# Performance work log

Measured on AMD Instinct MI355X. Metric: run time of the kernel, lower is better.

## Reference

```python
import jax, jax.numpy as jnp
import numpy as np

SR = 48000
MAX_DUR = 5.0
N_AUDIO = 480000  # 10 s @ 48 kHz
K_IR = int(SR * MAX_DUR)  # 240000 taps


def setup_inputs() -> dict:
    key = jax.random.key(0)
    k1, k2 = jax.random.split(key)
    audio = jax.random.normal(k1, (N_AUDIO,), dtype=jnp.float32)
    impulse_response = jax.random.normal(k2, (K_IR,), dtype=jnp.float32)
    return {"audio": audio, "impulse_response": impulse_response}


def reference(audio, impulse_response):
    # torch: pad audio with (K-1) zeros, then conv1d (= cross-correlation, no flip)
    K = impulse_response.shape[0]
    a_pad = jnp.concatenate([audio, jnp.zeros((K - 1,), dtype=audio.dtype)])
    # out[t] = sum_k a_pad[t+k] * ir[k], valid correlation -> length N
    out = jnp.correlate(a_pad, impulse_response, mode="valid")
    # trailing peak normalization
    return out / jnp.max(jnp.abs(out))
```

## Files before the change

kernel.cpp:

```cpp
#include <hip/hip_runtime.h>

typedef unsigned int u32;


constexpr int N_AUDIO = 480000;
constexpr int M_FFT   = 1048576;

constexpr size_t OFF_C0   = 0;
constexpr size_t OFF_C1   = (size_t)M_FFT * 8;
constexpr size_t OFF_SLOT = OFF_C1 + (size_t)M_FFT * 8;

#define SW(i) ((i) + ((i) >> 4))
constexpr int LSZ = 1088;

struct F2 { float x, y; };
constexpr double D_PI = 3.14159265358979323846264338327950288;
constexpr double tay_sin(double x) {
    double t = x, s = x, x2 = x * x;
    for (int k = 1; k <= 11; ++k) { t *= -x2 / (double)((2 * k) * (2 * k + 1)); s += t; }
    return s;
}
constexpr double tay_cos(double x) {
    double t = 1.0, s = 1.0, x2 = x * x;
    for (int k = 1; k <= 11; ++k) { t *= -x2 / (double)((2 * k - 1) * (2 * k)); s += t; }
    return s;
}
struct Tab { F2 v[1024]; };
constexpr Tab make_t1() {
    Tab tb{};
    for (int j = 0; j < 1024; ++j) {
        int jj = (j < 512) ? j : j - 1024;
        double a = -2.0 * D_PI * (double)jj / 1024.0;
        tb.v[j] = F2{(float)tay_cos(a), (float)tay_sin(a)};
    }
    return tb;
}
constexpr Tab make_t2() {
    Tab tb{};
    for (int j = 0; j < 1024; ++j) {
        double a = -2.0 * D_PI * (double)j / 1048576.0;
        tb.v[j] = F2{(float)tay_cos(a), (float)tay_sin(a)};
    }
    return tb;
}
__device__ constexpr Tab ROM_T1 = make_t1();
__device__ constexpr Tab ROM_T2 = make_t2();

__device__ __forceinline__ float2 ldrom(const Tab& tb, int i) {
    F2 f = tb.v[i];
    return make_float2(f.x, f.y);
}
__device__ __forceinline__ float2 cmul(float2 a, float2 b) {
    return make_float2(a.x * b.x - a.y * b.y, a.x * b.y + a.y * b.x);
}
__device__ __forceinline__ void stage_tabs(float2* lt1, float2* lt2, int t) {
    #pragma unroll
    for (int q = 0; q < 4; ++q) {
        int i = t + 256 * q;
        lt1[i] = ldrom(ROM_T1, i);
        lt2[i] = ldrom(ROM_T2, i);
    }
}

template<int R>
__device__ __forceinline__ void fft1024_r4(float2 (*A0)[LSZ], float2 (*B0)[LSZ],
                                           const float2* lt1, int t) {
    float2 (*A)[LSZ] = A0;
    float2 (*B)[LSZ] = B0;
    #pragma unroll
    for (int s = 0; s < 5; ++s) {
        const int L  = 1 << (2 * s);
        const int k  = t & (L - 1);
        const int p0 = 4 * t - 3 * k;
        const float2 w  = lt1[k << (9 - 2 * s)];
        const float2 w2 = lt1[k << (8 - 2 * s)];
        #pragma unroll
        for (int j = 0; j < R; ++j) {
            float2 x0 = A[j][SW(t)];
            float2 x2 = A[j][SW(t + 256)];
            float2 x1 = A[j][SW(t + 512)];
            float2 x3 = A[j][SW(t + 768)];
            float2 wx1 = cmul(w, x1), wx3 = cmul(w, x3);
            float2 u0 = make_float2(x0.x + wx1.x, x0.y + wx1.y);
            float2 u1 = make_float2(x0.x - wx1.x, x0.y - wx1.y);
            float2 u2 = make_float2(x2.x + wx3.x, x2.y + wx3.y);
            float2 u3 = make_float2(x2.x - wx3.x, x2.y - wx3.y);
            float2 a2 = cmul(w2, u2);
            float2 a3 = cmul(w2, u3);
            B[j][SW(p0)]         = make_float2(u0.x + a2.x, u0.y + a2.y);
            B[j][SW(p0 + L)]     = make_float2(u1.x + a3.y, u1.y - a3.x);
            B[j][SW(p0 + 2*L)]   = make_float2(u0.x - a2.x, u0.y - a2.y);
            B[j][SW(p0 + 3*L)]   = make_float2(u1.x - a3.y, u1.y + a3.x);
        }
        __syncthreads();
        float2 (*tmp)[LSZ] = A; A = B; B = tmp;
    }
}

__device__ __forceinline__ void fft512_r4(float2 (*A0)[LSZ], float2 (*B0)[LSZ],
                                          const float2* lt1, int t) {
    float2 (*A)[LSZ] = A0;
    float2 (*B)[LSZ] = B0;
    const int j  = t >> 7;
    const int tt = t & 127;
    #pragma unroll
    for (int s = 0; s < 4; ++s) {
        const int L  = 1 << (2 * s);
        const int k  = tt & (L - 1);
        const int p0 = 4 * tt - 3 * k;
        const float2 w  = lt1[k << (9 - 2 * s)];
        const float2 w2 = lt1[k << (8 - 2 * s)];
        float2 x0 = A[j][SW(tt)];
        float2 x2 = A[j][SW(tt + 128)];
        float2 x1 = A[j][SW(tt + 256)];
        float2 x3 = A[j][SW(tt + 384)];
        float2 wx1 = cmul(w, x1), wx3 = cmul(w, x3);
        float2 u0 = make_float2(x0.x + wx1.x, x0.y + wx1.y);
        float2 u1 = make_float2(x0.x - wx1.x, x0.y - wx1.y);
        float2 u2 = make_float2(x2.x + wx3.x, x2.y + wx3.y);
        float2 u3 = make_float2(x2.x - wx3.x, x2.y - wx3.y);
        float2 a2 = cmul(w2, u2);
        float2 a3 = cmul(w2, u3);
        B[j][SW(p0)]       = make_float2(u0.x + a2.x, u0.y + a2.y);
        B[j][SW(p0 + L)]   = make_float2(u1.x + a3.y, u1.y - a3.x);
        B[j][SW(p0 + 2*L)] = make_float2(u0.x - a2.x, u0.y - a2.y);
        B[j][SW(p0 + 3*L)] = make_float2(u1.x - a3.y, u1.y + a3.x);
        __syncthreads();
        float2 (*tmp)[LSZ] = A; A = B; B = tmp;
    }
    #pragma unroll
    for (int h = 0; h < 2; ++h) {
        int i = tt + 128 * h;
        float2 x0 = A[j][SW(i)];
        float2 x1 = A[j][SW(i + 256)];
        float2 w  = lt1[i << 1];
        float2 wx = cmul(w, x1);
        B[j][SW(i)]       = make_float2(x0.x + wx.x, x0.y + wx.y);
        B[j][SW(i + 256)] = make_float2(x0.x - wx.x, x0.y - wx.y);
    }
    __syncthreads();
}

__global__ __launch_bounds__(256) void kA(const float* __restrict__ a,
                                          const float* __restrict__ b,
                                          float2* __restrict__ outb,
                                          u32* __restrict__ slot) {
    __shared__ float2 buf0[1][LSZ], buf1[1][LSZ], lt1[1024], lt2[1024];
    const int t = threadIdx.x;
    const int r = blockIdx.x;
    if (r == 0 && t == 0) *slot = 0u;
    stage_tabs(lt1, lt2, t);
    #pragma unroll
    for (int q = 0; q < 4; ++q) {
        int c = t + 256 * q;
        int base = c * 1024 + r;
        float av = 0.f, bv = 0.f;
        if (c < 468 || (c == 468 && r < 768)) av = a[base];
        if (c < 234 || (c == 234 && r < 384)) bv = b[base];
        buf0[0][SW(c)] = make_float2(av, bv);
    }
    __syncthreads();
    fft1024_r4<1>(buf0, buf1, lt1, t);
    #pragma unroll
    for (int q = 0; q < 4; ++q) {
        int k1 = t + 256 * q;
        int e = r * k1;
        float2 w = cmul(lt1[e >> 10], lt2[e & 1023]);
        outb[r * 1024 + k1] = cmul(w, buf1[0][SW(k1)]);
    }
}

__global__ __launch_bounds__(256) void kBC(const float2* __restrict__ in,
                                           float2* __restrict__ gbuf) {
    __shared__ float2 buf0[2][LSZ], buf1[2][LSZ], lt1[1024], lt2[1024];
    const int t = threadIdx.x;
    const int bidx = blockIdx.x;
    const int cA = (bidx == 0) ? 0   : bidx;
    const int cB = (bidx == 0) ? 512 : 1024 - bidx;
    stage_tabs(lt1, lt2, t);
    #pragma unroll
    for (int q = 0; q < 4; ++q) {
        int r = t + 256 * q;
        buf0[0][SW(r)] = in[r * 1024 + cA];
        buf0[1][SW(r)] = in[r * 1024 + cB];
    }
    __syncthreads();
    fft1024_r4<2>(buf0, buf1, lt1, t);
    #pragma unroll
    for (int q = 0; q < 4; ++q) {
        int k2 = t + 256 * q;
        #pragma unroll
        for (int j = 0; j < 2; ++j) {
            float2 z1 = buf1[j][SW(k2)];
            float2 z2;
            if (bidx == 0) z2 = (j == 0) ? buf1[0][SW((1024 - k2) & 1023)]
                                         : buf1[1][SW(1023 - k2)];
            else           z2 = buf1[j ^ 1][SW(1023 - k2)];
            float2 Af  = make_float2(0.5f * (z1.x + z2.x), 0.5f * (z1.y - z2.y));
            float2 cBf = make_float2(0.5f * (z1.y + z2.y), 0.5f * (z1.x - z2.x));
            buf0[j][SW(k2)] = cmul(Af, cBf);
        }
    }
    __syncthreads();
    const float invN2 = 1.0f / 524288.0f;
    #pragma unroll
    for (int j = 0; j < 2; ++j) {
        const int bcol = (j == 0) ? cA : cB;
        const float2 wb = lt2[bcol];
        #pragma unroll
        for (int h = 0; h < 2; ++h) {
            int k2v = t + 256 * h;
            float2 z1 = buf0[j][SW(k2v)];
            int jr, p2;
            if (bidx == 0) { jr = j; p2 = (j == 0) ? (512 - k2v) : (511 - k2v); }
            else           { jr = j ^ 1; p2 = 511 - k2v; }
            float2 z2c = buf0[jr][SW(p2)];
            z2c.y = -z2c.y;
            float2 A2 = make_float2(0.5f * (z1.x + z2c.x), 0.5f * (z1.y + z2c.y));
            float2 D2 = make_float2(0.5f * (z1.x - z2c.x), 0.5f * (z1.y - z2c.y));
            float2 cw = cmul(lt1[k2v], wb);
            float2 iB = cmul(make_float2(cw.y, cw.x), D2);
            float2 Z  = make_float2(A2.x + iB.x, A2.y + iB.y);
            buf1[j][SW(k2v)] = make_float2(Z.x * invN2, -Z.y * invN2);
        }
    }
    __syncthreads();
    fft512_r4(buf1, buf0, lt1, t);
    const int jc = t >> 7, tt = t & 127;
    const int bcol = (jc == 0) ? cA : cB;
    #pragma unroll
    for (int u = 0; u < 4; ++u) {
        int k1 = tt + 128 * u;
        int e2 = 2 * bcol * k1;
        float2 w = cmul(lt1[e2 >> 10], lt2[e2 & 1023]);
        gbuf[bcol * 512 + k1] = cmul(w, buf0[jc][SW(k1)]);
    }
}

__global__ __launch_bounds__(256) void kD(const float2* __restrict__ gbuf,
                                          float2* __restrict__ rawT2,
                                          u32* __restrict__ slot) {
    __shared__ float2 buf0[1][LSZ], buf1[1][LSZ], lt1[1024];
    __shared__ float wmax[4];
    const int t = threadIdx.x;
    const int col = blockIdx.x;
    #pragma unroll
    for (int q = 0; q < 4; ++q) { int i = t + 256 * q; lt1[i] = ldrom(ROM_T1, i); }
    #pragma unroll
    for (int q = 0; q < 4; ++q) {
        int b = t + 256 * q;
        buf0[0][SW(b)] = gbuf[(size_t)b * 512 + col];
    }
    __syncthreads();
    fft1024_r4<1>(buf0, buf1, lt1, t);
    float m = 0.0f;
    #pragma unroll
    for (int q = 0; q < 4; ++q) {
        int k2 = t + 256 * q;
        int to = 2 * col + 1024 * k2;
        if (to < N_AUDIO) {
            float2 v = buf1[0][SW(k2)];
            rawT2[col * 1024 + k2] = make_float2(v.x, -v.y);
            m = fmaxf(m, fmaxf(fabsf(v.x), fabsf(v.y)));
        }
    }
    for (int off = 32; off > 0; off >>= 1) m = fmaxf(m, __shfl_down(m, off, 64));
    if ((t & 63) == 0) wmax[t >> 6] = m;
    __syncthreads();
    if (t == 0) {
        float bm = fmaxf(fmaxf(wmax[0], wmax[1]), fmaxf(wmax[2], wmax[3]));
        atomicMax(slot, __float_as_uint(bm));
    }
}

__global__ __launch_bounds__(256) void kE(const float2* __restrict__ rawT2,
                                          const u32* __restrict__ slot,
                                          float* __restrict__ out) {
    __shared__ float2 tile[32][33];
    const int t  = threadIdx.x;
    const int K0 = (blockIdx.x & 15) * 32;
    const int Q0 = (blockIdx.x >> 4) * 32;
    #pragma unroll
    for (int i = 0; i < 4; ++i) {
        int idx = t + 256 * i;
        int row = idx >> 5, col = idx & 31;
        tile[col][row] = rawT2[(size_t)(K0 + row) * 1024 + Q0 + col];
    }
    __syncthreads();
    const float inv = 1.0f / __uint_as_float(*slot);
    #pragma unroll
    for (int i = 0; i < 4; ++i) {
        int idx = t + 256 * i;
        int cc = idx >> 5, rr = idx & 31;
        int o = (Q0 + cc) * 1024 + 2 * (K0 + rr);
        if (o < N_AUDIO) {
            float2 v = tile[cc][rr];
            *(float2*)(out + o) = make_float2(v.x * inv, v.y * inv);
        }
    }
}

extern "C" void kernel_launch(void* const* d_in, const int* in_sizes, int n_in,
                              void* d_out, int out_size, void* d_ws, size_t ws_size,
                              hipStream_t stream) {
    const float* audio = (const float*)d_in[0];
    const float* ir    = (const float*)d_in[1];
    float* out = (float*)d_out;

    char* ws = (char*)d_ws;
    float2* cb0 = (float2*)(ws + OFF_C0);
    float2* cb1 = (float2*)(ws + OFF_C1);
    u32*    slot = (u32*)(ws + OFF_SLOT);

    kA<<<1024, 256, 0, stream>>>(audio, ir, cb1, slot);
    kBC<<<512, 256, 0, stream>>>(cb1, cb0);
    kD<<<512, 256, 0, stream>>>(cb0, cb1, slot);
    kE<<<512, 256, 0, stream>>>((const float2*)cb1, slot, out);
}
```

Before: 99.03 us.

## Fuse final normalization into kD via grid-wide spin barrier, drop kE

```diff
diff --git a/kernel.cpp b/kernel.cpp
--- a/kernel.cpp
+++ b/kernel.cpp
@@ -9,6 +9,7 @@
 constexpr size_t OFF_C0   = 0;
 constexpr size_t OFF_C1   = (size_t)M_FFT * 8;
 constexpr size_t OFF_SLOT = OFF_C1 + (size_t)M_FFT * 8;
+constexpr size_t OFF_CNT  = OFF_SLOT + 4;
 
 #define SW(i) ((i) + ((i) >> 4))
 constexpr int LSZ = 1088;
@@ -144,11 +145,12 @@
 __global__ __launch_bounds__(256) void kA(const float* __restrict__ a,
                                           const float* __restrict__ b,
                                           float2* __restrict__ outb,
-                                          u32* __restrict__ slot) {
+                                          u32* __restrict__ slot,
+                                          u32* __restrict__ cnt) {
     __shared__ float2 buf0[1][LSZ], buf1[1][LSZ], lt1[1024], lt2[1024];
     const int t = threadIdx.x;
     const int r = blockIdx.x;
-    if (r == 0 && t == 0) *slot = 0u;
+    if (r == 0 && t == 0) { *slot = 0u; *cnt = 0u; }
     stage_tabs(lt1, lt2, t);
     #pragma unroll
     for (int q = 0; q < 4; ++q) {
@@ -238,30 +240,35 @@
 }
 
 __global__ __launch_bounds__(256) void kD(const float2* __restrict__ gbuf,
-                                          float2* __restrict__ rawT2,
-                                          u32* __restrict__ slot) {
-    __shared__ float2 buf0[1][LSZ], buf1[1][LSZ], lt1[1024];
+                                          u32* __restrict__ slot,
+                                          u32* __restrict__ cnt,
+                                          float* __restrict__ out) {
+    __shared__ float2 buf0[2][LSZ], buf1[2][LSZ], lt1[1024];
     __shared__ float wmax[4];
+    __shared__ float s_inv;
     const int t = threadIdx.x;
-    const int col = blockIdx.x;
+    const int qb = blockIdx.x;
     #pragma unroll
     for (int q = 0; q < 4; ++q) { int i = t + 256 * q; lt1[i] = ldrom(ROM_T1, i); }
     #pragma unroll
     for (int q = 0; q < 4; ++q) {
         int b = t + 256 * q;
-        buf0[0][SW(b)] = gbuf[(size_t)b * 512 + col];
-    }
-    __syncthreads();
-    fft1024_r4<1>(buf0, buf1, lt1, t);
+        float4 v = *(const float4*)(gbuf + (size_t)b * 512 + 2 * qb);
+        buf0[0][SW(b)] = make_float2(v.x, v.y);
+        buf0[1][SW(b)] = make_float2(v.z, v.w);
+    }
+    __syncthreads();
+    fft1024_r4<2>(buf0, buf1, lt1, t);
+    float2 r0[4], r1[4];
     float m = 0.0f;
     #pragma unroll
     for (int q = 0; q < 4; ++q) {
         int k2 = t + 256 * q;
-        int to = 2 * col + 1024 * k2;
-        if (to < N_AUDIO) {
-            float2 v = buf1[0][SW(k2)];
-            rawT2[col * 1024 + k2] = make_float2(v.x, -v.y);
-            m = fmaxf(m, fmaxf(fabsf(v.x), fabsf(v.y)));
+        r0[q] = buf1[0][SW(k2)];
+        r1[q] = buf1[1][SW(k2)];
+        if (k2 < 468 || (k2 == 468 && qb < 192)) {
+            m = fmaxf(m, fmaxf(fabsf(r0[q].x), fabsf(r0[q].y)));
+            m = fmaxf(m, fmaxf(fabsf(r1[q].x), fabsf(r1[q].y)));
         }
     }
     for (int off = 32; off > 0; off >>= 1) m = fmaxf(m, __shfl_down(m, off, 64));
@@ -270,32 +277,23 @@
     if (t == 0) {
         float bm = fmaxf(fmaxf(wmax[0], wmax[1]), fmaxf(wmax[2], wmax[3]));
         atomicMax(slot, __float_as_uint(bm));
-    }
-}
-
-__global__ __launch_bounds__(256) void kE(const float2* __restrict__ rawT2,
-                                          const u32* __restrict__ slot,
-                                          float* __restrict__ out) {
-    __shared__ float2 tile[32][33];
-    const int t  = threadIdx.x;
-    const int K0 = (blockIdx.x & 15) * 32;
-    const int Q0 = (blockIdx.x >> 4) * 32;
-    #pragma unroll
-    for (int i = 0; i < 4; ++i) {
-        int idx = t + 256 * i;
-        int row = idx >> 5, col = idx & 31;
-        tile[col][row] = rawT2[(size_t)(K0 + row) * 1024 + Q0 + col];
-    }
-    __syncthreads();
-    const float inv = 1.0f / __uint_as_float(*slot);
-    #pragma unroll
-    for (int i = 0; i < 4; ++i) {
-        int idx = t + 256 * i;
-        int cc = idx >> 5, rr = idx & 31;
-        int o = (Q0 + cc) * 1024 + 2 * (K0 + rr);
-        if (o < N_AUDIO) {
-            float2 v = tile[cc][rr];
-            *(float2*)(out + o) = make_float2(v.x * inv, v.y * inv);
+        __threadfence();
+        atomicAdd(cnt, 1u);
+        while (atomicAdd(cnt, 0u) < 256u) {
+            __builtin_amdgcn_s_sleep(2);
+        }
+        __threadfence();
+        s_inv = 1.0f / __uint_as_float(atomicAdd(slot, 0u));
+    }
+    __syncthreads();
+    const float inv = s_inv;
+    #pragma unroll
+    for (int q = 0; q < 4; ++q) {
+        int k2 = t + 256 * q;
+        if (k2 < 468 || (k2 == 468 && qb < 192)) {
+            float4 o = make_float4(r0[q].x * inv, -r0[q].y * inv,
+                                   r1[q].x * inv, -r1[q].y * inv);
+            *(float4*)(out + 1024 * k2 + 4 * qb) = o;
         }
     }
 }
@@ -311,9 +309,9 @@
     float2* cb0 = (float2*)(ws + OFF_C0);
     float2* cb1 = (float2*)(ws + OFF_C1);
     u32*    slot = (u32*)(ws + OFF_SLOT);
-
-    kA<<<1024, 256, 0, stream>>>(audio, ir, cb1, slot);
+    u32*    cnt  = (u32*)(ws + OFF_CNT);
+
+    kA<<<1024, 256, 0, stream>>>(audio, ir, cb1, slot, cnt);
     kBC<<<512, 256, 0, stream>>>(cb1, cb0);
-    kD<<<512, 256, 0, stream>>>(cb0, cb1, slot);
-    kE<<<512, 256, 0, stream>>>((const float2*)cb1, slot, out);
-}
+    kD<<<256, 256, 0, stream>>>(cb0, slot, cnt, out);
+}
```

After: 110.1 us. 1.11x slower.
